# Optimization experiments

Measured on AMD Instinct MI355X. Metric: run time of the kernel, lower is better.

Reference implementation:

```python
import jax, jax.numpy as jnp
import numpy as np

B, N, K, H = 8192, 512, 8, 1024  # batch, size_half, n_segments, hidden width


def setup_inputs() -> dict:
    key = jax.random.key(0)
    ks = jax.random.split(key, 8)
    out_dim = N * (2 * K + 1)  # 8704
    v_in = jax.random.uniform(ks[0], (B, 2 * N), jnp.float32)  # in [0,1]
    log_density = jax.random.uniform(ks[1], (B, 1), jnp.float32)
    W1 = jax.random.normal(ks[2], (N, H), jnp.float32) / np.float32(np.sqrt(N))
    b1 = jnp.zeros((H,), jnp.float32)
    W2 = jax.random.normal(ks[3], (H, H), jnp.float32) / np.float32(np.sqrt(H))
    b2 = jnp.zeros((H,), jnp.float32)
    W3 = jax.random.normal(ks[4], (H, out_dim), jnp.float32) / np.float32(np.sqrt(H))
    b3 = jnp.zeros((out_dim,), jnp.float32)
    return {"v_in": v_in, "log_density": log_density,
            "W1": W1, "b1": b1, "W2": W2, "b2": b2, "W3": W3, "b3": b3}


def reference(v_in, log_density, W1, b1, W2, b2, W3, b3):
    v_passive = v_in[:, :N]   # even_sites=True -> passive first
    v_active = v_in[:, N:]
    # fully connected net, tanh on every layer (no_final_activation=False)
    x = jnp.tanh((v_passive - 0.5) @ W1 + b1)
    x = jnp.tanh(x @ W2 + b2)
    x = jnp.tanh(x @ W3 + b3)
    net = x.reshape(B, N, 2 * K + 1)
    h_net, w_net = net[..., : K + 1], net[..., K + 1 :]
    w_norm = jax.nn.softmax(w_net, axis=2)                          # (B,N,K)
    eh = jnp.exp(h_net)                                             # (B,N,K+1)
    denom = (0.5 * w_norm * (eh[..., :-1] + eh[..., 1:])).sum(axis=2, keepdims=True)
    h_norm = eh / denom                                             # (B,N,K+1)
    zeros = jnp.zeros((B, N, 1), v_in.dtype)
    knots_x = jnp.concatenate([zeros, jnp.cumsum(w_norm, axis=2)], axis=2)  # (B,N,K+1)
    knots_y = jnp.concatenate(
        [zeros, jnp.cumsum(0.5 * w_norm * (h_norm[..., :-1] + h_norm[..., 1:]), axis=2)],
        axis=2)                                                     # (B,N,K+1)
    # left-searchsorted(knots_x, v_active) == count of knots strictly below v
    k = jnp.clip(jnp.sum(knots_x < v_active[..., None], axis=2) - 1, 0, K - 1)  # (B,N)
    idx = k[..., None]
    w_seg = jnp.take_along_axis(w_norm, idx, axis=2)[..., 0]
    h_lo = jnp.take_along_axis(h_norm, idx, axis=2)[..., 0]
    h_hi = jnp.take_along_axis(h_norm, idx + 1, axis=2)[..., 0]
    x_lo = jnp.take_along_axis(knots_x, idx, axis=2)[..., 0]
    y_lo = jnp.take_along_axis(knots_y, idx, axis=2)[..., 0]
    alpha = (v_active - x_lo) / w_seg
    v_active_out = y_lo + alpha * h_lo * w_seg + 0.5 * alpha ** 2 * (h_hi - h_lo) * w_seg
    v_out = jnp.concatenate([v_passive, v_active_out], axis=1)      # (B,2N)
    log_density_out = log_density - jnp.log(h_lo + alpha * (h_hi - h_lo)).sum(axis=1, keepdims=True)
    return v_out, log_density_out
```

## Files before the change

kernel.cpp:

```cpp
#include <hip/hip_runtime.h>
#include <math.h>

#define BB    8192
#define NN    512
#define KKN   8
#define HH    1024
#define OUTD  (NN * (2 * KKN + 1))

typedef unsigned short ushort_t;
typedef __bf16 bf16x8 __attribute__((ext_vector_type(8)));
typedef float  f32x4  __attribute__((ext_vector_type(4)));

__device__ inline ushort_t f2bf(float f) {
    unsigned int u = __float_as_uint(f);
    unsigned int r = (u + 0x7fffu + ((u >> 16) & 1u)) >> 16;
    return (ushort_t)r;
}
__device__ inline float bf2f(ushort_t u) {
    return __uint_as_float(((unsigned int)u) << 16);
}

__global__ __launch_bounds__(256) void conv_v(
    const float* __restrict__ v_in, ushort_t* __restrict__ a0b)
{
    int t = blockIdx.x * 256 + threadIdx.x;
    int e0 = t * 2;
    int b = e0 >> 9;
    int n = e0 & 511;
    const float2 v = *(const float2*)(v_in + (size_t)b * (2 * NN) + n);
    ushort_t* o = a0b + (size_t)b * NN + n;
    o[0] = f2bf(v.x - 0.5f);
    o[1] = f2bf(v.y - 0.5f);
}

__global__ __launch_bounds__(256) void transpose_cvt(
    const float* __restrict__ W, ushort_t* __restrict__ WT, int Kd, int Nd)
{
    __shared__ float tile[32][33];
    const int bx = blockIdx.x * 32;
    const int by = blockIdx.y * 32;
    const int tx = threadIdx.x;
    const int ty = threadIdx.y;
#pragma unroll
    for (int i = 0; i < 32; i += 8)
        tile[ty + i][tx] = W[(size_t)(by + ty + i) * Nd + bx + tx];
    __syncthreads();
#pragma unroll
    for (int i = 0; i < 32; i += 8)
        WT[(size_t)(bx + ty + i) * Kd + by + tx] = f2bf(tile[tx][ty + i]);
}

__global__ __launch_bounds__(256) void gemm_bt_tanh(
    const ushort_t* __restrict__ A,
    const ushort_t* __restrict__ BT,
    const float* __restrict__ bias,
    ushort_t* __restrict__ C,
    int M, int N_, int K)
{
    __shared__ __align__(16) ushort_t sA[128 * 32];
    __shared__ __align__(16) ushort_t sB[128 * 32];

    const int t    = threadIdx.x;
    const int lane = t & 63;
    const int w    = t >> 6;
    const int wy   = w >> 1;
    const int wx   = w & 1;
    const int quad = lane >> 4;
    const int l16  = lane & 15;

    const int brow = blockIdx.y * 128;
    const int bcol = blockIdx.x * 128;

    f32x4 acc[4][4] = {};

    const int cwb = (t & ~63);

    for (int k0 = 0; k0 < K; k0 += 32) {
        __syncthreads();
#pragma unroll
        for (int p = 0; p < 2; ++p) {
            const int c  = p * 256 + t;
            const int cb = p * 256 + cwb;
            const ushort_t* ga = A  + (size_t)(brow + (c >> 2)) * K + k0 + (c & 3) * 8;
            const ushort_t* gb = BT + (size_t)(bcol + (c >> 2)) * K + k0 + (c & 3) * 8;
            __builtin_amdgcn_global_load_lds(
                (const __attribute__((address_space(1))) void*)ga,
                (__attribute__((address_space(3))) void*)(sA + (size_t)cb * 8), 16, 0, 0);
            __builtin_amdgcn_global_load_lds(
                (const __attribute__((address_space(1))) void*)gb,
                (__attribute__((address_space(3))) void*)(sB + (size_t)cb * 8), 16, 0, 0);
        }
        __syncthreads();

        bf16x8 af[4], bfr[4];
#pragma unroll
        for (int i = 0; i < 4; ++i) {
            af[i]  = *(const bf16x8*)(sA + (wy * 64 + i * 16 + l16) * 32 + quad * 8);
            bfr[i] = *(const bf16x8*)(sB + (wx * 64 + i * 16 + l16) * 32 + quad * 8);
        }
#pragma unroll
        for (int i = 0; i < 4; ++i)
#pragma unroll
            for (int j = 0; j < 4; ++j)
                acc[i][j] = __builtin_amdgcn_mfma_f32_16x16x32_bf16(
                    af[i], bfr[j], acc[i][j], 0, 0, 0);
    }

    const int row0 = brow + wy * 64;
    const int col0 = bcol + wx * 64;
#pragma unroll
    for (int i = 0; i < 4; ++i) {
#pragma unroll
        for (int j = 0; j < 4; ++j) {
            const int col = col0 + j * 16 + l16;
            const float bv = bias[col];
#pragma unroll
            for (int r = 0; r < 4; ++r) {
                const int row = row0 + i * 16 + quad * 4 + r;
                C[(size_t)row * N_ + col] = f2bf(tanhf(acc[i][j][r] + bv));
            }
        }
    }
}

__global__ __launch_bounds__(512) void spline_post(
    const ushort_t* __restrict__ net,
    const float* __restrict__ v_in,
    const float* __restrict__ ld_in,
    float* __restrict__ v_out,
    float* __restrict__ ld_out)
{
    const int b = blockIdx.x;
    const int n = threadIdx.x;

    __shared__ __align__(16) ushort_t srow[OUTD];
    __shared__ float wred[8];

    {
        const float4* g = (const float4*)(net + (size_t)b * OUTD);
        float4* s = (float4*)srow;
        for (int i = n; i < OUTD * 2 / 16; i += 512) s[i] = g[i];
    }
    __syncthreads();

    float t17[17];
#pragma unroll
    for (int i = 0; i < 17; i++) t17[i] = bf2f(srow[n * 17 + i]);

    float m = t17[9];
#pragma unroll
    for (int i = 10; i < 17; i++) m = fmaxf(m, t17[i]);
    float wn[8], wsum = 0.f;
#pragma unroll
    for (int i = 0; i < 8; i++) { wn[i] = expf(t17[9 + i] - m); wsum += wn[i]; }
    const float winv = 1.f / wsum;
#pragma unroll
    for (int i = 0; i < 8; i++) wn[i] *= winv;

    float eh[9];
#pragma unroll
    for (int i = 0; i < 9; i++) eh[i] = expf(t17[i]);
    float denom = 0.f;
#pragma unroll
    for (int k = 0; k < 8; k++) denom += 0.5f * wn[k] * (eh[k] + eh[k + 1]);
    const float dinv = 1.f / denom;
    float hn[9];
#pragma unroll
    for (int i = 0; i < 9; i++) hn[i] = eh[i] * dinv;

    float kx[9], ky[9];
    kx[0] = 0.f; ky[0] = 0.f;
#pragma unroll
    for (int k = 0; k < 8; k++) {
        kx[k + 1] = kx[k] + wn[k];
        ky[k + 1] = ky[k] + 0.5f * wn[k] * (hn[k] + hn[k + 1]);
    }

    const float va = v_in[(size_t)b * (2 * NN) + NN + n];

    int cnt = 0;
#pragma unroll
    for (int j = 0; j < 9; j++) cnt += (kx[j] < va) ? 1 : 0;
    int k = cnt - 1;
    k = k < 0 ? 0 : (k > KKN - 1 ? KKN - 1 : k);

    const float wseg = wn[k];
    const float hlo = hn[k], hhi = hn[k + 1];
    const float xlo = kx[k], ylo = ky[k];
    const float alpha = (va - xlo) / wseg;
    const float vact = ylo + alpha * hlo * wseg + 0.5f * alpha * alpha * (hhi - hlo) * wseg;
    float lt = logf(hlo + alpha * (hhi - hlo));

    v_out[(size_t)b * (2 * NN) + n]      = v_in[(size_t)b * (2 * NN) + n];
    v_out[(size_t)b * (2 * NN) + NN + n] = vact;

#pragma unroll
    for (int o = 32; o > 0; o >>= 1) lt += __shfl_down(lt, o, 64);
    if ((n & 63) == 0) wred[n >> 6] = lt;
    __syncthreads();
    if (n == 0) {
        float s = 0.f;
#pragma unroll
        for (int i = 0; i < 8; i++) s += wred[i];
        ld_out[b] = ld_in[b] - s;
    }
}

extern "C" void kernel_launch(void* const* d_in, const int* in_sizes, int n_in,
                              void* d_out, int out_size, void* d_ws, size_t ws_size,
                              hipStream_t stream)
{
    const float* v_in = (const float*)d_in[0];
    const float* ld   = (const float*)d_in[1];
    const float* W1   = (const float*)d_in[2];
    const float* b1   = (const float*)d_in[3];
    const float* W2   = (const float*)d_in[4];
    const float* b2   = (const float*)d_in[5];
    const float* W3   = (const float*)d_in[6];
    const float* b3   = (const float*)d_in[7];

    float* out    = (float*)d_out;
    float* v_out  = out;
    float* ld_out = out + (size_t)BB * (2 * NN);

    const size_t Mi = 1048576;
    int    chunk;
    size_t region;
    if      (ws_size >= 172 * Mi) { chunk = 8192; region = 136 * Mi; }
    else if (ws_size >= 104 * Mi) { chunk = 4096; region =  68 * Mi; }
    else if (ws_size >=  70 * Mi) { chunk = 2048; region =  34 * Mi; }
    else                          { chunk = 1024; region =  24 * Mi; }

    char* ws = (char*)d_ws;
    ushort_t* a0b = (ushort_t*)(ws);
    ushort_t* x1b = (ushort_t*)(ws + 8 * Mi);
    ushort_t* netc = (ushort_t*)(ws);
    ushort_t* x2b = (ushort_t*)(ws + region);
    ushort_t* W1T = (ushort_t*)(ws + region + 16 * Mi);
    ushort_t* W2T = (ushort_t*)(ws + region + 17 * Mi);
    ushort_t* W3T = (ushort_t*)(ws + region + 19 * Mi);

    conv_v<<<dim3(BB * NN / 2 / 256), dim3(256), 0, stream>>>(v_in, a0b);
    transpose_cvt<<<dim3(HH / 32, NN / 32),   dim3(32, 8), 0, stream>>>(W1, W1T, NN, HH);
    transpose_cvt<<<dim3(HH / 32, HH / 32),   dim3(32, 8), 0, stream>>>(W2, W2T, HH, HH);
    transpose_cvt<<<dim3(OUTD / 32, HH / 32), dim3(32, 8), 0, stream>>>(W3, W3T, HH, OUTD);

    gemm_bt_tanh<<<dim3(HH / 128, BB / 128), dim3(256), 0, stream>>>(
        a0b, W1T, b1, x1b, BB, HH, NN);
    gemm_bt_tanh<<<dim3(HH / 128, BB / 128), dim3(256), 0, stream>>>(
        x1b, W2T, b2, x2b, BB, HH, HH);

    for (int c = 0; c < BB / chunk; ++c) {
        const ushort_t* xa = x2b + (size_t)c * chunk * HH;
        gemm_bt_tanh<<<dim3(OUTD / 128, chunk / 128), dim3(256), 0, stream>>>(
            xa, W3T, b3, netc, chunk, OUTD, HH);
        spline_post<<<dim3(chunk), dim3(512), 0, stream>>>(
            netc,
            v_in   + (size_t)c * chunk * (2 * NN),
            ld     + (size_t)c * chunk,
            v_out  + (size_t)c * chunk * (2 * NN),
            ld_out + (size_t)c * chunk);
    }
}
```

Before: 444.9 us.

## Permute W3 output columns for coalesced spline reads and use fast tanh/exp

```diff
diff --git a/kernel.cpp b/kernel.cpp
--- a/kernel.cpp
+++ b/kernel.cpp
@@ -18,6 +18,12 @@
 }
 __device__ inline float bf2f(ushort_t u) {
     return __uint_as_float(((unsigned int)u) << 16);
+}
+
+__device__ inline float fast_tanh(float x) {
+    float xc = fminf(fmaxf(x, -10.f), 10.f);
+    float t  = __expf(2.f * xc);
+    return (t - 1.f) * __builtin_amdgcn_rcpf(t + 1.f);
 }
 
 __global__ __launch_bounds__(256) void conv_v(
@@ -33,6 +39,7 @@
     o[1] = f2bf(v.y - 0.5f);
 }
 
+template <bool PERM>
 __global__ __launch_bounds__(256) void transpose_cvt(
     const float* __restrict__ W, ushort_t* __restrict__ WT, int Kd, int Nd)
 {
@@ -46,10 +53,14 @@
         tile[ty + i][tx] = W[(size_t)(by + ty + i) * Nd + bx + tx];
     __syncthreads();
 #pragma unroll
-    for (int i = 0; i < 32; i += 8)
-        WT[(size_t)(bx + ty + i) * Kd + by + tx] = f2bf(tile[tx][ty + i]);
-}
-
+    for (int i = 0; i < 32; i += 8) {
+        int r = bx + ty + i;
+        if (PERM) r = (r % 17) * 512 + (r / 17);
+        WT[(size_t)r * Kd + by + tx] = f2bf(tile[tx][ty + i]);
+    }
+}
+
+template <bool PERM_BIAS>
 __global__ __launch_bounds__(256) void gemm_bt_tanh(
     const ushort_t* __restrict__ A,
     const ushort_t* __restrict__ BT,
@@ -113,17 +124,18 @@
 #pragma unroll
         for (int j = 0; j < 4; ++j) {
             const int col = col0 + j * 16 + l16;
-            const float bv = bias[col];
+            const int bidx = PERM_BIAS ? ((col & 511) * 17 + (col >> 9)) : col;
+            const float bv = bias[bidx];
 #pragma unroll
             for (int r = 0; r < 4; ++r) {
                 const int row = row0 + i * 16 + quad * 4 + r;
-                C[(size_t)row * N_ + col] = f2bf(tanhf(acc[i][j][r] + bv));
+                C[(size_t)row * N_ + col] = f2bf(fast_tanh(acc[i][j][r] + bv));
             }
         }
     }
 }
 
-__global__ __launch_bounds__(512) void spline_post(
+__global__ __launch_bounds__(256) void spline_post(
     const ushort_t* __restrict__ net,
     const float* __restrict__ v_in,
     const float* __restrict__ ld_in,
@@ -131,79 +143,83 @@
     float* __restrict__ ld_out)
 {
     const int b = blockIdx.x;
-    const int n = threadIdx.x;
-
-    __shared__ __align__(16) ushort_t srow[OUTD];
-    __shared__ float wred[8];
+    const int t = threadIdx.x;
+
+    unsigned int pl[17];
+    const ushort_t* base = net + (size_t)b * OUTD + 2 * t;
+#pragma unroll
+    for (int p = 0; p < 17; ++p)
+        pl[p] = *(const unsigned int*)(base + p * 512);
 
     {
-        const float4* g = (const float4*)(net + (size_t)b * OUTD);
-        float4* s = (float4*)srow;
-        for (int i = n; i < OUTD * 2 / 16; i += 512) s[i] = g[i];
-    }
+        const float2 vp = *(const float2*)(v_in + (size_t)b * (2 * NN) + 2 * t);
+        *(float2*)(v_out + (size_t)b * (2 * NN) + 2 * t) = vp;
+    }
+    const float2 va2 = *(const float2*)(v_in + (size_t)b * (2 * NN) + NN + 2 * t);
+
+    float vact[2];
+    float lt_sum = 0.f;
+#pragma unroll 1
+    for (int u = 0; u < 2; ++u) {
+        const int sh = u * 16;
+        float t17[17];
+#pragma unroll
+        for (int p = 0; p < 17; ++p)
+            t17[p] = bf2f((ushort_t)(pl[p] >> sh));
+
+        float m = t17[9];
+#pragma unroll
+        for (int i = 10; i < 17; i++) m = fmaxf(m, t17[i]);
+        float wn[8], wsum = 0.f;
+#pragma unroll
+        for (int i = 0; i < 8; i++) { wn[i] = __expf(t17[9 + i] - m); wsum += wn[i]; }
+        const float winv = 1.f / wsum;
+#pragma unroll
+        for (int i = 0; i < 8; i++) wn[i] *= winv;
+
+        float eh[9];
+#pragma unroll
+        for (int i = 0; i < 9; i++) eh[i] = __expf(t17[i]);
+        float denom = 0.f;
+#pragma unroll
+        for (int k = 0; k < 8; k++) denom += 0.5f * wn[k] * (eh[k] + eh[k + 1]);
+        const float dinv = 1.f / denom;
+        float hn[9];
+#pragma unroll
+        for (int i = 0; i < 9; i++) hn[i] = eh[i] * dinv;
+
+        float kx[9], ky[9];
+        kx[0] = 0.f; ky[0] = 0.f;
+#pragma unroll
+        for (int k = 0; k < 8; k++) {
+            kx[k + 1] = kx[k] + wn[k];
+            ky[k + 1] = ky[k] + 0.5f * wn[k] * (hn[k] + hn[k + 1]);
+        }
+
+        const float va = (u == 0) ? va2.x : va2.y;
+        int cnt = 0;
+#pragma unroll
+        for (int j = 0; j < 9; j++) cnt += (kx[j] < va) ? 1 : 0;
+        int k = cnt - 1;
+        k = k < 0 ? 0 : (k > KKN - 1 ? KKN - 1 : k);
+
+        const float wseg = wn[k];
+        const float hlo = hn[k], hhi = hn[k + 1];
+        const float xlo = kx[k], ylo = ky[k];
+        const float alpha = (va - xlo) / wseg;
+        vact[u] = ylo + alpha * hlo * wseg + 0.5f * alpha * alpha * (hhi - hlo) * wseg;
+        lt_sum += logf(hlo + alpha * (hhi - hlo));
+    }
+
+    *(float2*)(v_out + (size_t)b * (2 * NN) + NN + 2 * t) = make_float2(vact[0], vact[1]);
+
+    __shared__ float wred[4];
+#pragma unroll
+    for (int o = 32; o > 0; o >>= 1) lt_sum += __shfl_down(lt_sum, o, 64);
+    if ((t & 63) == 0) wred[t >> 6] = lt_sum;
     __syncthreads();
-
-    float t17[17];
-#pragma unroll
-    for (int i = 0; i < 17; i++) t17[i] = bf2f(srow[n * 17 + i]);
-
-    float m = t17[9];
-#pragma unroll
-    for (int i = 10; i < 17; i++) m = fmaxf(m, t17[i]);
-    float wn[8], wsum = 0.f;
-#pragma unroll
-    for (int i = 0; i < 8; i++) { wn[i] = expf(t17[9 + i] - m); wsum += wn[i]; }
-    const float winv = 1.f / wsum;
-#pragma unroll
-    for (int i = 0; i < 8; i++) wn[i] *= winv;
-
-    float eh[9];
-#pragma unroll
-    for (int i = 0; i < 9; i++) eh[i] = expf(t17[i]);
-    float denom = 0.f;
-#pragma unroll
-    for (int k = 0; k < 8; k++) denom += 0.5f * wn[k] * (eh[k] + eh[k + 1]);
-    const float dinv = 1.f / denom;
-    float hn[9];
-#pragma unroll
-    for (int i = 0; i < 9; i++) hn[i] = eh[i] * dinv;
-
-    float kx[9], ky[9];
-    kx[0] = 0.f; ky[0] = 0.f;
-#pragma unroll
-    for (int k = 0; k < 8; k++) {
-        kx[k + 1] = kx[k] + wn[k];
-        ky[k + 1] = ky[k] + 0.5f * wn[k] * (hn[k] + hn[k + 1]);
-    }
-
-    const float va = v_in[(size_t)b * (2 * NN) + NN + n];
-
-    int cnt = 0;
-#pragma unroll
-    for (int j = 0; j < 9; j++) cnt += (kx[j] < va) ? 1 : 0;
-    int k = cnt - 1;
-    k = k < 0 ? 0 : (k > KKN - 1 ? KKN - 1 : k);
-
-    const float wseg = wn[k];
-    const float hlo = hn[k], hhi = hn[k + 1];
-    const float xlo = kx[k], ylo = ky[k];
-    const float alpha = (va - xlo) / wseg;
-    const float vact = ylo + alpha * hlo * wseg + 0.5f * alpha * alpha * (hhi - hlo) * wseg;
-    float lt = logf(hlo + alpha * (hhi - hlo));
-
-    v_out[(size_t)b * (2 * NN) + n]      = v_in[(size_t)b * (2 * NN) + n];
-    v_out[(size_t)b * (2 * NN) + NN + n] = vact;
-
-#pragma unroll
-    for (int o = 32; o > 0; o >>= 1) lt += __shfl_down(lt, o, 64);
-    if ((n & 63) == 0) wred[n >> 6] = lt;
-    __syncthreads();
-    if (n == 0) {
-        float s = 0.f;
-#pragma unroll
-        for (int i = 0; i < 8; i++) s += wred[i];
-        ld_out[b] = ld_in[b] - s;
-    }
+    if (t == 0)
+        ld_out[b] = ld_in[b] - (wred[0] + wred[1] + wred[2] + wred[3]);
 }
 
 extern "C" void kernel_launch(void* const* d_in, const int* in_sizes, int n_in,
@@ -241,20 +257,20 @@
     ushort_t* W3T = (ushort_t*)(ws + region + 19 * Mi);
 
     conv_v<<<dim3(BB * NN / 2 / 256), dim3(256), 0, stream>>>(v_in, a0b);
-    transpose_cvt<<<dim3(HH / 32, NN / 32),   dim3(32, 8), 0, stream>>>(W1, W1T, NN, HH);
-    transpose_cvt<<<dim3(HH / 32, HH / 32),   dim3(32, 8), 0, stream>>>(W2, W2T, HH, HH);
-    transpose_cvt<<<dim3(OUTD / 32, HH / 32), dim3(32, 8), 0, stream>>>(W3, W3T, HH, OUTD);
-
-    gemm_bt_tanh<<<dim3(HH / 128, BB / 128), dim3(256), 0, stream>>>(
+    transpose_cvt<false><<<dim3(HH / 32, NN / 32),   dim3(32, 8), 0, stream>>>(W1, W1T, NN, HH);
+    transpose_cvt<false><<<dim3(HH / 32, HH / 32),   dim3(32, 8), 0, stream>>>(W2, W2T, HH, HH);
+    transpose_cvt<true ><<<dim3(OUTD / 32, HH / 32), dim3(32, 8), 0, stream>>>(W3, W3T, HH, OUTD);
+
+    gemm_bt_tanh<false><<<dim3(HH / 128, BB / 128), dim3(256), 0, stream>>>(
         a0b, W1T, b1, x1b, BB, HH, NN);
-    gemm_bt_tanh<<<dim3(HH / 128, BB / 128), dim3(256), 0, stream>>>(
+    gemm_bt_tanh<false><<<dim3(HH / 128, BB / 128), dim3(256), 0, stream>>>(
         x1b, W2T, b2, x2b, BB, HH, HH);
 
     for (int c = 0; c < BB / chunk; ++c) {
         const ushort_t* xa = x2b + (size_t)c * chunk * HH;
-        gemm_bt_tanh<<<dim3(OUTD / 128, chunk / 128), dim3(256), 0, stream>>>(
+        gemm_bt_tanh<true><<<dim3(OUTD / 128, chunk / 128), dim3(256), 0, stream>>>(
             xa, W3T, b3, netc, chunk, OUTD, HH);
-        spline_post<<<dim3(chunk), dim3(512), 0, stream>>>(
+        spline_post<<<dim3(chunk), dim3(256), 0, stream>>>(
             netc,
             v_in   + (size_t)c * chunk * (2 * NN),
             ld     + (size_t)c * chunk,
```

Result: faster. 431.7 us (-3.0%).
